# Optimization experiments

Measured on AMD Instinct MI355X. Metric: run time of the kernel, lower is better.

The kernel has to match this reference:

```python
import jax, jax.numpy as jnp
import numpy as np

EPS_F = 1e-6   # epsilon_F global in original repo
GAMMA = 0.8
K = 5
BN_EPS = 1e-5
M = 128
N = 100000
E = 1600000
MY = 10

def setup_inputs() -> dict:
    key = jax.random.key(0)
    ks = jax.random.split(key, 6)
    X = jax.random.normal(ks[0], (M, N), dtype=jnp.float32)
    # xavier_uniform for F: limit = sqrt(6/(m+m))
    lim = float(np.sqrt(6.0 / (M + M)))
    F_mat = jax.random.uniform(ks[1], (M, M), dtype=jnp.float32, minval=-lim, maxval=lim)
    B = (1.0 / np.sqrt(M)) * jax.random.normal(ks[2], (MY, M), dtype=jnp.float32)
    bn_weight = jnp.ones((M,), dtype=jnp.float32)
    bn_bias = jnp.zeros((M,), dtype=jnp.float32)
    edge_val = jax.random.uniform(ks[3], (E,), dtype=jnp.float32)
    edge_row = jax.random.randint(ks[4], (E,), 0, N, dtype=jnp.int64 if jax.config.jax_enable_x64 else jnp.int32)
    edge_col = jax.random.randint(ks[5], (E,), 0, N, dtype=jnp.int64 if jax.config.jax_enable_x64 else jnp.int32)
    return {"X": X, "F_mat": F_mat, "B": B, "bn_weight": bn_weight,
            "bn_bias": bn_bias, "edge_val": edge_val,
            "edge_row": edge_row, "edge_col": edge_col}

def reference(X, F_mat, B, bn_weight, bn_bias, edge_val, edge_row, edge_col):
    n = X.shape[1]
    # normalized Gram matrix g(F) = F^T F / (||F^T F||_fro + eps)
    FF = F_mat.T @ F_mat                       # [m, m]
    G = FF / (jnp.linalg.norm(FF) + EPS_F)
    X_first = X                                # [m, n]

    def step(Xc, _):
        Y = Xc.T                               # [n, m]
        # SpMM: (S_t @ Y)[r] += val * Y[c]
        SY = jax.ops.segment_sum(edge_val[:, None] * Y[edge_col], edge_row,
                                 num_segments=n)   # [n, m]
        Xn = GAMMA * (G @ SY.T) + X_first          # [m, n]
        return Xn, None

    Xk, _ = jax.lax.scan(step, X, None, length=K)
    out = Xk.T                                 # [n, m]
    # BatchNorm1d over feature dim (training-mode batch stats); dropout omitted (eval)
    mu = out.mean(axis=0)
    var = out.var(axis=0)
    out = (out - mu) * jax.lax.rsqrt(var + BN_EPS) * bn_weight + bn_bias
    return out @ B.T                           # [n, m_y]
```

## Files before the change

kernel.cpp:

```cpp
#include <hip/hip_runtime.h>
#include <math.h>

#define MDIM 128
#define MY 10
#define GAMMA 0.8f
#define KITER 5
#define NPASS 8

__device__ __forceinline__ float bf2f(unsigned short h) {
    return __uint_as_float(((unsigned int)h) << 16);
}
__device__ __forceinline__ unsigned short f2bf(float f) {
    unsigned int u = __float_as_uint(f);
    u += 0x7fffu + ((u >> 16) & 1u);
    return (unsigned short)(u >> 16);
}

__global__ void k_transpose(const float* __restrict__ X, float* __restrict__ Y0,
                            unsigned short* __restrict__ Y0h,
                            unsigned short* __restrict__ Yh0, int n) {
    __shared__ float tile[32][33];
    int r0 = blockIdx.x * 32;
    int f0 = blockIdx.y * 32;
    int tx = threadIdx.x, ty = threadIdx.y;
    #pragma unroll
    for (int i = 0; i < 32; i += 8) {
        tile[ty + i][tx] = X[(size_t)(f0 + ty + i) * n + (r0 + tx)];
    }
    __syncthreads();
    #pragma unroll
    for (int i = 0; i < 32; i += 8) {
        float v = tile[tx][ty + i];
        unsigned short h = f2bf(v);
        Y0[(size_t)(r0 + ty + i) * MDIM + (f0 + tx)] = v;
        Y0h[(size_t)(r0 + ty + i) * MDIM + (f0 + tx)] = h;
        Yh0[(size_t)(r0 + ty + i) * MDIM + (f0 + tx)] = h;
    }
}

__global__ void k_gram(const float* __restrict__ F, float* __restrict__ FF,
                       float* __restrict__ normAcc) {
    int i = blockIdx.x, j = threadIdx.x;
    float acc = 0.f;
    for (int k = 0; k < MDIM; ++k)
        acc = fmaf(F[k * MDIM + i], F[k * MDIM + j], acc);
    FF[i * MDIM + j] = acc;
    __shared__ float red[MDIM];
    red[j] = acc * acc;
    __syncthreads();
    for (int s = 64; s > 0; s >>= 1) {
        if (j < s) red[j] += red[j + s];
        __syncthreads();
    }
    if (j == 0) atomicAdd(normAcc, red[0]);
}

__global__ void k_gnorm(const float* __restrict__ FF, const float* __restrict__ normAcc,
                        float* __restrict__ G) {
    int idx = blockIdx.x * 256 + threadIdx.x;
    float s = GAMMA / (sqrtf(*normAcc) + 1e-6f);
    G[idx] = FF[idx] * s;
}

__global__ void k_hist(const int* __restrict__ erow, int* __restrict__ cnt, int E) {
    int e = blockIdx.x * 256 + threadIdx.x;
    if (e < E) atomicAdd(&cnt[erow[e]], 1);
}

__global__ void k_scan1(const int* __restrict__ cnt, int* __restrict__ blockSums, int n) {
    int tid = threadIdx.x;
    int base = blockIdx.x * 1024 + tid * 4;
    int s = 0;
    if (base + 3 < n) {
        int4 v = *(const int4*)&cnt[base];
        s = v.x + v.y + v.z + v.w;
    } else {
        for (int i = 0; i < 4; ++i)
            if (base + i < n) s += cnt[base + i];
    }
    __shared__ int red[256];
    red[tid] = s;
    __syncthreads();
    for (int st = 128; st > 0; st >>= 1) {
        if (tid < st) red[tid] += red[tid + st];
        __syncthreads();
    }
    if (tid == 0) blockSums[blockIdx.x] = red[0];
}

__global__ void k_scan2(int* __restrict__ blockSums, int* __restrict__ row_off,
                        int nb, int n) {
    __shared__ int s[256];
    int tid = threadIdx.x;
    int v = (tid < nb) ? blockSums[tid] : 0;
    s[tid] = v;
    __syncthreads();
    for (int off = 1; off < 256; off <<= 1) {
        int t = (tid >= off) ? s[tid - off] : 0;
        __syncthreads();
        s[tid] += t;
        __syncthreads();
    }
    if (tid < nb) blockSums[tid] = s[tid] - v;
    if (tid == 0) row_off[n] = s[255];
}

__global__ void k_scan3(const int* __restrict__ cnt, const int* __restrict__ blockOff,
                        int* __restrict__ row_off, int n) {
    int tid = threadIdx.x;
    int base = blockIdx.x * 1024 + tid * 4;
    int v[4];
    #pragma unroll
    for (int i = 0; i < 4; ++i) v[i] = (base + i < n) ? cnt[base + i] : 0;
    int local = v[0] + v[1] + v[2] + v[3];
    __shared__ int s[256];
    s[tid] = local;
    __syncthreads();
    for (int off = 1; off < 256; off <<= 1) {
        int t = (tid >= off) ? s[tid - off] : 0;
        __syncthreads();
        s[tid] += t;
        __syncthreads();
    }
    int excl = s[tid] - local + blockOff[blockIdx.x];
    #pragma unroll
    for (int i = 0; i < 4; ++i) {
        if (base + i < n) { row_off[base + i] = excl; excl += v[i]; }
    }
}

__global__ void k_scatter(const int* __restrict__ erow, const int* __restrict__ ecol,
                          const float* __restrict__ eval_, int* __restrict__ cursor,
                          int2* __restrict__ csr_cv, int E, int rlo, int rhi) {
    int e = blockIdx.x * 256 + threadIdx.x;
    if (e < E) {
        int r = erow[e];
        if (r >= rlo && r < rhi) {
            int pos = atomicAdd(&cursor[r], 1);
            csr_cv[pos] = make_int2(ecol[e] << 8, __float_as_int(eval_[e]));
        }
    }
}

__global__ void __launch_bounds__(256, 8) k_fused(const unsigned short* __restrict__ Yh,
                                                  const int* __restrict__ row_off,
                                                  const int2* __restrict__ csr_cv,
                                                  const float* __restrict__ G,
                                                  const float* __restrict__ Y0,
                                                  const unsigned short* __restrict__ Y0h,
                                                  float* __restrict__ Yout,
                                                  unsigned short* __restrict__ Yhout,
                                                  float* __restrict__ stats,
                                                  int writeH, int writeF, int n) {
    __shared__ float sSY[32 * MDIM];
    int tid = threadIdx.x;
    int ty = tid >> 5;
    int tx = tid & 31;
    int rbase = blockIdx.x * 32;
    const char* yb = (const char*)Yh;
    int lbo = tx * 8;

    for (int i = 0; i < 4; ++i) {
        int rloc = ty * 4 + i;
        int e0 = row_off[rbase + rloc];
        int e1 = row_off[rbase + rloc + 1];
        float4 a = make_float4(0.f, 0.f, 0.f, 0.f);
        int e = e0;
        for (; e + 8 <= e1; e += 8) {
            int2 p0 = csr_cv[e + 0];
            int2 p1 = csr_cv[e + 1];
            int2 p2 = csr_cv[e + 2];
            int2 p3 = csr_cv[e + 3];
            int2 p4 = csr_cv[e + 4];
            int2 p5 = csr_cv[e + 5];
            int2 p6 = csr_cv[e + 6];
            int2 p7 = csr_cv[e + 7];
            ushort4 h0 = *(const ushort4*)(yb + (size_t)(p0.x + lbo));
            ushort4 h1 = *(const ushort4*)(yb + (size_t)(p1.x + lbo));
            ushort4 h2 = *(const ushort4*)(yb + (size_t)(p2.x + lbo));
            ushort4 h3 = *(const ushort4*)(yb + (size_t)(p3.x + lbo));
            ushort4 h4 = *(const ushort4*)(yb + (size_t)(p4.x + lbo));
            ushort4 h5 = *(const ushort4*)(yb + (size_t)(p5.x + lbo));
            ushort4 h6 = *(const ushort4*)(yb + (size_t)(p6.x + lbo));
            ushort4 h7 = *(const ushort4*)(yb + (size_t)(p7.x + lbo));
            float v0 = __int_as_float(p0.y);
            float v1 = __int_as_float(p1.y);
            float v2 = __int_as_float(p2.y);
            float v3 = __int_as_float(p3.y);
            float v4 = __int_as_float(p4.y);
            float v5 = __int_as_float(p5.y);
            float v6 = __int_as_float(p6.y);
            float v7 = __int_as_float(p7.y);
            a.x = fmaf(v0, bf2f(h0.x), a.x);
            a.y = fmaf(v0, bf2f(h0.y), a.y);
            a.z = fmaf(v0, bf2f(h0.z), a.z);
            a.w = fmaf(v0, bf2f(h0.w), a.w);
            a.x = fmaf(v1, bf2f(h1.x), a.x);
            a.y = fmaf(v1, bf2f(h1.y), a.y);
            a.z = fmaf(v1, bf2f(h1.z), a.z);
            a.w = fmaf(v1, bf2f(h1.w), a.w);
            a.x = fmaf(v2, bf2f(h2.x), a.x);
            a.y = fmaf(v2, bf2f(h2.y), a.y);
            a.z = fmaf(v2, bf2f(h2.z), a.z);
            a.w = fmaf(v2, bf2f(h2.w), a.w);
            a.x = fmaf(v3, bf2f(h3.x), a.x);
            a.y = fmaf(v3, bf2f(h3.y), a.y);
            a.z = fmaf(v3, bf2f(h3.z), a.z);
            a.w = fmaf(v3, bf2f(h3.w), a.w);
            a.x = fmaf(v4, bf2f(h4.x), a.x);
            a.y = fmaf(v4, bf2f(h4.y), a.y);
            a.z = fmaf(v4, bf2f(h4.z), a.z);
            a.w = fmaf(v4, bf2f(h4.w), a.w);
            a.x = fmaf(v5, bf2f(h5.x), a.x);
            a.y = fmaf(v5, bf2f(h5.y), a.y);
            a.z = fmaf(v5, bf2f(h5.z), a.z);
            a.w = fmaf(v5, bf2f(h5.w), a.w);
            a.x = fmaf(v6, bf2f(h6.x), a.x);
            a.y = fmaf(v6, bf2f(h6.y), a.y);
            a.z = fmaf(v6, bf2f(h6.z), a.z);
            a.w = fmaf(v6, bf2f(h6.w), a.w);
            a.x = fmaf(v7, bf2f(h7.x), a.x);
            a.y = fmaf(v7, bf2f(h7.y), a.y);
            a.z = fmaf(v7, bf2f(h7.z), a.z);
            a.w = fmaf(v7, bf2f(h7.w), a.w);
        }
        for (; e + 4 <= e1; e += 4) {
            int2 p0 = csr_cv[e + 0];
            int2 p1 = csr_cv[e + 1];
            int2 p2 = csr_cv[e + 2];
            int2 p3 = csr_cv[e + 3];
            ushort4 h0 = *(const ushort4*)(yb + (size_t)(p0.x + lbo));
            ushort4 h1 = *(const ushort4*)(yb + (size_t)(p1.x + lbo));
            ushort4 h2 = *(const ushort4*)(yb + (size_t)(p2.x + lbo));
            ushort4 h3 = *(const ushort4*)(yb + (size_t)(p3.x + lbo));
            float v0 = __int_as_float(p0.y);
            float v1 = __int_as_float(p1.y);
            float v2 = __int_as_float(p2.y);
            float v3 = __int_as_float(p3.y);
            a.x = fmaf(v0, bf2f(h0.x), a.x);
            a.y = fmaf(v0, bf2f(h0.y), a.y);
            a.z = fmaf(v0, bf2f(h0.z), a.z);
            a.w = fmaf(v0, bf2f(h0.w), a.w);
            a.x = fmaf(v1, bf2f(h1.x), a.x);
            a.y = fmaf(v1, bf2f(h1.y), a.y);
            a.z = fmaf(v1, bf2f(h1.z), a.z);
            a.w = fmaf(v1, bf2f(h1.w), a.w);
            a.x = fmaf(v2, bf2f(h2.x), a.x);
            a.y = fmaf(v2, bf2f(h2.y), a.y);
            a.z = fmaf(v2, bf2f(h2.z), a.z);
            a.w = fmaf(v2, bf2f(h2.w), a.w);
            a.x = fmaf(v3, bf2f(h3.x), a.x);
            a.y = fmaf(v3, bf2f(h3.y), a.y);
            a.z = fmaf(v3, bf2f(h3.z), a.z);
            a.w = fmaf(v3, bf2f(h3.w), a.w);
        }
        for (; e < e1; ++e) {
            int2 p = csr_cv[e];
            float v = __int_as_float(p.y);
            ushort4 h = *(const ushort4*)(yb + (size_t)(p.x + lbo));
            a.x = fmaf(v, bf2f(h.x), a.x);
            a.y = fmaf(v, bf2f(h.y), a.y);
            a.z = fmaf(v, bf2f(h.z), a.z);
            a.w = fmaf(v, bf2f(h.w), a.w);
        }
        *(float4*)&sSY[rloc * MDIM + tx * 4] = a;
    }

    size_t r0 = (size_t)rbase + ty * 4;
    int f0 = tx * 4;
    float4 acc[4];
    #pragma unroll
    for (int i = 0; i < 4; ++i) acc[i] = make_float4(0.f, 0.f, 0.f, 0.f);

    for (int j = 0; j < MDIM; j += 4) {
        float4 g0 = *(const float4*)&G[(j + 0) * MDIM + f0];
        float4 g1 = *(const float4*)&G[(j + 1) * MDIM + f0];
        float4 g2 = *(const float4*)&G[(j + 2) * MDIM + f0];
        float4 g3 = *(const float4*)&G[(j + 3) * MDIM + f0];
        #pragma unroll
        for (int i = 0; i < 4; ++i) {
            float4 sr = *(const float4*)&sSY[(ty * 4 + i) * MDIM + j];
            acc[i].x = fmaf(sr.x, g0.x, acc[i].x);
            acc[i].y = fmaf(sr.x, g0.y, acc[i].y);
            acc[i].z = fmaf(sr.x, g0.z, acc[i].z);
            acc[i].w = fmaf(sr.x, g0.w, acc[i].w);
            acc[i].x = fmaf(sr.y, g1.x, acc[i].x);
            acc[i].y = fmaf(sr.y, g1.y, acc[i].y);
            acc[i].z = fmaf(sr.y, g1.z, acc[i].z);
            acc[i].w = fmaf(sr.y, g1.w, acc[i].w);
            acc[i].x = fmaf(sr.z, g2.x, acc[i].x);
            acc[i].y = fmaf(sr.z, g2.y, acc[i].y);
            acc[i].z = fmaf(sr.z, g2.z, acc[i].z);
            acc[i].w = fmaf(sr.z, g2.w, acc[i].w);
            acc[i].x = fmaf(sr.w, g3.x, acc[i].x);
            acc[i].y = fmaf(sr.w, g3.y, acc[i].y);
            acc[i].z = fmaf(sr.w, g3.z, acc[i].z);
            acc[i].w = fmaf(sr.w, g3.w, acc[i].w);
        }
    }

    float4 bs = make_float4(0.f, 0.f, 0.f, 0.f);
    float4 bq = make_float4(0.f, 0.f, 0.f, 0.f);
    #pragma unroll
    for (int i = 0; i < 4; ++i) {
        float4 y0;
        if (writeF) {
            y0 = *(const float4*)&Y0[(r0 + i) * MDIM + f0];
        } else {
            ushort4 t = *(const ushort4*)&Y0h[(r0 + i) * MDIM + f0];
            y0.x = bf2f(t.x);
            y0.y = bf2f(t.y);
            y0.z = bf2f(t.z);
            y0.w = bf2f(t.w);
        }
        float4 o;
        o.x = acc[i].x + y0.x;
        o.y = acc[i].y + y0.y;
        o.z = acc[i].z + y0.z;
        o.w = acc[i].w + y0.w;
        if (writeF) {
            *(float4*)&Yout[(r0 + i) * MDIM + f0] = o;
            bs.x += o.x; bs.y += o.y; bs.z += o.z; bs.w += o.w;
            bq.x = fmaf(o.x, o.x, bq.x);
            bq.y = fmaf(o.y, o.y, bq.y);
            bq.z = fmaf(o.z, o.z, bq.z);
            bq.w = fmaf(o.w, o.w, bq.w);
        }
        if (writeH) {
            ushort4 h;
            h.x = f2bf(o.x);
            h.y = f2bf(o.y);
            h.z = f2bf(o.z);
            h.w = f2bf(o.w);
            *(ushort4*)&Yhout[(r0 + i) * MDIM + f0] = h;
        }
    }

    if (writeF) {
        __syncthreads();
        *(float4*)&sSY[ty * MDIM + f0] = bs;
        *(float4*)&sSY[8 * MDIM + ty * MDIM + f0] = bq;
        __syncthreads();
        if (tid < MDIM) {
            float a = 0.f, b = 0.f;
            #pragma unroll
            for (int t = 0; t < 8; ++t) {
                a += sSY[t * MDIM + tid];
                b += sSY[8 * MDIM + t * MDIM + tid];
            }
            atomicAdd(&stats[tid], a);
            atomicAdd(&stats[MDIM + tid], b);
        }
    }
}

__global__ void k_finalize(const float* __restrict__ stats, const float* __restrict__ B,
                           const float* __restrict__ bnw, const float* __restrict__ bnb,
                           float* __restrict__ Bs, float* __restrict__ cvec, int n) {
    int f = threadIdx.x;
    float inv_n = 1.f / (float)n;
    float mu = stats[f] * inv_n;
    float var = stats[MDIM + f] * inv_n - mu * mu;
    float rs = rsqrtf(var + 1e-5f);
    float sw = rs * bnw[f];
    float cv = bnb[f] - mu * sw;
    __shared__ float red[MDIM];
    for (int o = 0; o < MY; ++o) {
        float b = B[o * MDIM + f];
        Bs[o * MDIM + f] = b * sw;
        red[f] = b * cv;
        __syncthreads();
        for (int s = 64; s > 0; s >>= 1) {
            if (f < s) red[f] += red[f + s];
            __syncthreads();
        }
        if (f == 0) cvec[o] = red[0];
        __syncthreads();
    }
}

__global__ void __launch_bounds__(256) k_project(const float* __restrict__ Y,
                                                 const float* __restrict__ Bs,
                                                 const float* __restrict__ cvec,
                                                 float* __restrict__ out, int n) {
    __shared__ float yt[16 * 129];
    __shared__ float sB[MY * 129];
    __shared__ float sc[MY];
    int tid = threadIdx.x;
    size_t rbase = (size_t)blockIdx.x * 16;
    for (int idx = tid; idx < 16 * MDIM; idx += 256) {
        int r = idx >> 7, f = idx & 127;
        yt[r * 129 + f] = Y[(rbase + r) * MDIM + f];
    }
    for (int idx = tid; idx < MY * MDIM; idx += 256) {
        int o = idx >> 7, f = idx & 127;
        sB[o * 129 + f] = Bs[idx];
    }
    if (tid < MY) sc[tid] = cvec[tid];
    __syncthreads();
    if (tid < 16 * MY) {
        int r = tid / MY, o = tid % MY;
        float acc = sc[o];
        for (int f = 0; f < MDIM; ++f)
            acc = fmaf(yt[r * 129 + f], sB[o * 129 + f], acc);
        out[(rbase + r) * MY + o] = acc;
    }
}

extern "C" void kernel_launch(void* const* d_in, const int* in_sizes, int n_in,
                              void* d_out, int out_size, void* d_ws, size_t ws_size,
                              hipStream_t stream) {
    const float* X    = (const float*)d_in[0];
    const float* F    = (const float*)d_in[1];
    const float* B    = (const float*)d_in[2];
    const float* bnw  = (const float*)d_in[3];
    const float* bnb  = (const float*)d_in[4];
    const float* ev   = (const float*)d_in[5];
    const int*   erow = (const int*)d_in[6];
    const int*   ecol = (const int*)d_in[7];
    float* out = (float*)d_out;
    const int n = in_sizes[0] / MDIM;
    const int E = in_sizes[5];

    char* w = (char*)d_ws;
    size_t off = 0;
    auto carve = [&](size_t bytes) -> void* {
        void* p = w + off;
        off += (bytes + 255) & ~(size_t)255;
        return p;
    };
    float*          Y0    = (float*)carve((size_t)n * MDIM * 4);
    float*          Ycur  = (float*)carve((size_t)n * MDIM * 4);
    unsigned short* Y0h   = (unsigned short*)carve((size_t)n * MDIM * 2);
    unsigned short* Yh_a  = (unsigned short*)carve((size_t)n * MDIM * 2);
    unsigned short* Yh_b  = (unsigned short*)carve((size_t)n * MDIM * 2);
    float* FF        = (float*)carve(MDIM * MDIM * 4);
    float* G         = (float*)carve(MDIM * MDIM * 4);
    int2*  csr_cv    = (int2*)carve((size_t)E * 8);
    int*   row_off   = (int*)carve((size_t)(n + 1) * 4);
    int*   cursor    = (int*)carve((size_t)n * 4);
    int*   cnt       = (int*)carve((size_t)n * 4);
    int*   blockSums = (int*)carve(1024 * 4);
    float* normAcc   = (float*)carve(4);
    float* stats     = (float*)carve(2 * MDIM * 4);
    float* Bs        = (float*)carve(MY * MDIM * 4);
    float* cvec      = (float*)carve(MY * 4);
    (void)ws_size;

    hipMemsetAsync(cnt, 0, (size_t)n * 4, stream);
    hipMemsetAsync(normAcc, 0, 4, stream);
    hipMemsetAsync(stats, 0, 2 * MDIM * 4, stream);

    k_transpose<<<dim3(n / 32, MDIM / 32), dim3(32, 8), 0, stream>>>(X, Y0, Y0h, Yh_a, n);
    k_gram<<<MDIM, MDIM, 0, stream>>>(F, FF, normAcc);
    k_gnorm<<<MDIM * MDIM / 256, 256, 0, stream>>>(FF, normAcc, G);

    const int nb = (n + 1023) / 1024;
    k_hist<<<(E + 255) / 256, 256, 0, stream>>>(erow, cnt, E);
    k_scan1<<<nb, 256, 0, stream>>>(cnt, blockSums, n);
    k_scan2<<<1, 256, 0, stream>>>(blockSums, row_off, nb, n);
    k_scan3<<<nb, 256, 0, stream>>>(cnt, blockSums, row_off, n);
    hipMemcpyAsync(cursor, row_off, (size_t)n * 4, hipMemcpyDeviceToDevice, stream);
    const int rstep = (n + NPASS - 1) / NPASS;
    for (int p = 0; p < NPASS; ++p) {
        int rlo = p * rstep;
        int rhi = rlo + rstep;
        if (rhi > n) rhi = n;
        k_scatter<<<(E + 255) / 256, 256, 0, stream>>>(erow, ecol, ev, cursor,
                                                       csr_cv, E, rlo, rhi);
    }

    for (int k = 0; k < KITER; ++k) {
        const unsigned short* hin = (k & 1) ? Yh_b : Yh_a;
        unsigned short*       hout = (k & 1) ? Yh_a : Yh_b;
        int writeH = (k < KITER - 1) ? 1 : 0;
        int writeF = (k == KITER - 1) ? 1 : 0;
        k_fused<<<n / 32, 256, 0, stream>>>(hin, row_off, csr_cv, G, Y0, Y0h, Ycur, hout,
                                            stats, writeH, writeF, n);
    }

    k_finalize<<<1, MDIM, 0, stream>>>(stats, B, bnw, bnb, Bs, cvec, n);
    k_project<<<n / 16, 256, 0, stream>>>(Ycur, Bs, cvec, out, n);
}
```

Baseline: 929.5 us.

## Replace multi-pass CSR scatter with two-level bucketed scatter

The CSR build used to run eight full passes over all edges, each placing only the edges whose row falls in a range. It now does one bucketing pass into 128-row buckets in a staging buffer, then a per-bucket placement kernel that writes final CSR positions from a localized range. This removes seven redundant reads of the edge arrays and should make the final scattered writes more cache-local. The cost is an extra staging buffer of E int2 and heavy atomic traffic on the bucket cursors. The fused kernel's grid size also changes to a ceiling division.

```diff
diff --git a/kernel.cpp b/kernel.cpp
--- a/kernel.cpp
+++ b/kernel.cpp
@@ -5,7 +5,8 @@
 #define MY 10
 #define GAMMA 0.8f
 #define KITER 5
-#define NPASS 8
+#define BSHIFT 7
+#define NBUCK(n) (((n) + 127) >> 7)
 
 __device__ __forceinline__ float bf2f(unsigned short h) {
     return __uint_as_float(((unsigned int)h) << 16);
@@ -129,16 +130,40 @@
     }
 }
 
-__global__ void k_scatter(const int* __restrict__ erow, const int* __restrict__ ecol,
-                          const float* __restrict__ eval_, int* __restrict__ cursor,
-                          int2* __restrict__ csr_cv, int E, int rlo, int rhi) {
+__global__ void k_binit(const int* __restrict__ row_off, int* __restrict__ bucketBase,
+                        int* __restrict__ bucketCursor, int nbk, int n) {
+    int b = blockIdx.x * 256 + threadIdx.x;
+    if (b <= nbk) {
+        int r = b << BSHIFT;
+        if (r > n) r = n;
+        int v = row_off[r];
+        bucketBase[b] = v;
+        if (b < nbk) bucketCursor[b] = v;
+    }
+}
+
+__global__ void k_bucket(const int* __restrict__ erow, const int* __restrict__ ecol,
+                         const float* __restrict__ eval_, int* __restrict__ bucketCursor,
+                         int2* __restrict__ stage, int E) {
     int e = blockIdx.x * 256 + threadIdx.x;
     if (e < E) {
         int r = erow[e];
-        if (r >= rlo && r < rhi) {
-            int pos = atomicAdd(&cursor[r], 1);
-            csr_cv[pos] = make_int2(ecol[e] << 8, __float_as_int(eval_[e]));
-        }
+        int c = ecol[e];
+        int pos = atomicAdd(&bucketCursor[r >> BSHIFT], 1);
+        stage[pos] = make_int2((c << BSHIFT) | (r & 127), __float_as_int(eval_[e]));
+    }
+}
+
+__global__ void k_place(const int2* __restrict__ stage, const int* __restrict__ bucketBase,
+                        int* __restrict__ cursor, int2* __restrict__ csr_cv) {
+    int b = blockIdx.x;
+    int lo = bucketBase[b], hi = bucketBase[b + 1];
+    int rbase = b << BSHIFT;
+    for (int e = lo + threadIdx.x; e < hi; e += 256) {
+        int2 s = stage[e];
+        int r = rbase + (s.x & 127);
+        int pos = atomicAdd(&cursor[r], 1);
+        csr_cv[pos] = make_int2((s.x >> BSHIFT) << 8, s.y);
     }
 }
 
@@ -307,11 +332,11 @@
         if (writeF) {
             y0 = *(const float4*)&Y0[(r0 + i) * MDIM + f0];
         } else {
-            ushort4 t = *(const ushort4*)&Y0h[(r0 + i) * MDIM + f0];
-            y0.x = bf2f(t.x);
-            y0.y = bf2f(t.y);
-            y0.z = bf2f(t.z);
-            y0.w = bf2f(t.w);
+            ushort4 t4 = *(const ushort4*)&Y0h[(r0 + i) * MDIM + f0];
+            y0.x = bf2f(t4.x);
+            y0.y = bf2f(t4.y);
+            y0.z = bf2f(t4.z);
+            y0.w = bf2f(t4.w);
         }
         float4 o;
         o.x = acc[i].x + y0.x;
@@ -421,6 +446,7 @@
     float* out = (float*)d_out;
     const int n = in_sizes[0] / MDIM;
     const int E = in_sizes[5];
+    const int nbk = NBUCK(n);
 
     char* w = (char*)d_ws;
     size_t off = 0;
@@ -437,10 +463,13 @@
     float* FF        = (float*)carve(MDIM * MDIM * 4);
     float* G         = (float*)carve(MDIM * MDIM * 4);
     int2*  csr_cv    = (int2*)carve((size_t)E * 8);
+    int2*  stage     = (int2*)carve((size_t)E * 8);
     int*   row_off   = (int*)carve((size_t)(n + 1) * 4);
     int*   cursor    = (int*)carve((size_t)n * 4);
     int*   cnt       = (int*)carve((size_t)n * 4);
     int*   blockSums = (int*)carve(1024 * 4);
+    int*   bucketBase   = (int*)carve((size_t)(nbk + 1) * 4);
+    int*   bucketCursor = (int*)carve((size_t)nbk * 4);
     float* normAcc   = (float*)carve(4);
     float* stats     = (float*)carve(2 * MDIM * 4);
     float* Bs        = (float*)carve(MY * MDIM * 4);
@@ -460,23 +489,18 @@
     k_scan1<<<nb, 256, 0, stream>>>(cnt, blockSums, n);
     k_scan2<<<1, 256, 0, stream>>>(blockSums, row_off, nb, n);
     k_scan3<<<nb, 256, 0, stream>>>(cnt, blockSums, row_off, n);
+    k_binit<<<(nbk + 256) / 256, 256, 0, stream>>>(row_off, bucketBase, bucketCursor, nbk, n);
     hipMemcpyAsync(cursor, row_off, (size_t)n * 4, hipMemcpyDeviceToDevice, stream);
-    const int rstep = (n + NPASS - 1) / NPASS;
-    for (int p = 0; p < NPASS; ++p) {
-        int rlo = p * rstep;
-        int rhi = rlo + rstep;
-        if (rhi > n) rhi = n;
-        k_scatter<<<(E + 255) / 256, 256, 0, stream>>>(erow, ecol, ev, cursor,
-                                                       csr_cv, E, rlo, rhi);
-    }
+    k_bucket<<<(E + 255) / 256, 256, 0, stream>>>(erow, ecol, ev, bucketCursor, stage, E);
+    k_place<<<nbk, 256, 0, stream>>>(stage, bucketBase, cursor, csr_cv);
 
     for (int k = 0; k < KITER; ++k) {
         const unsigned short* hin = (k & 1) ? Yh_b : Yh_a;
         unsigned short*       hout = (k & 1) ? Yh_a : Yh_b;
         int writeH = (k < KITER - 1) ? 1 : 0;
         int writeF = (k == KITER - 1) ? 1 : 0;
-        k_fused<<<n / 32, 256, 0, stream>>>(hin, row_off, csr_cv, G, Y0, Y0h, Ycur, hout,
-                                            stats, writeH, writeF, n);
+        k_fused<<<(n + 31) / 32, 256, 0, stream>>>(hin, row_off, csr_cv, G, Y0, Y0h,
+                                                   Ycur, hout, stats, writeH, writeF, n);
     }
 
     k_finalize<<<1, MDIM, 0, stream>>>(stats, B, bnw, bnb, Bs, cvec, n);
```

Measured after the change: 1.243 ms. 1.34x slower.

## Single-pass CSR scatter, drop fp32 output buffer, project from bf16, nontemporal edge loads

Applied to the files above, without the earlier changes.

Replaces the eight range-filtered scatter passes with one scatter pass and initializes the cursor inside the scan kernel, removing the device copy. The final iteration no longer writes an fp32 output; the projection reads the bf16 buffer instead. Edge-list loads in the SpMM use nontemporal hints. This cuts repeated edge reads and output traffic, at the cost of bf16 precision in the projection input and less locality in scatter atomics.

```diff
diff --git a/kernel.cpp b/kernel.cpp
--- a/kernel.cpp
+++ b/kernel.cpp
@@ -5,7 +5,6 @@
 #define MY 10
 #define GAMMA 0.8f
 #define KITER 5
-#define NPASS 8
 
 __device__ __forceinline__ float bf2f(unsigned short h) {
     return __uint_as_float(((unsigned int)h) << 16);
@@ -14,6 +13,13 @@
     unsigned int u = __float_as_uint(f);
     u += 0x7fffu + ((u >> 16) & 1u);
     return (unsigned short)(u >> 16);
+}
+__device__ __forceinline__ int2 ldnt(const int2* p) {
+    long long v = __builtin_nontemporal_load((const long long*)p);
+    int2 r;
+    r.x = (int)(v & 0xFFFFFFFFLL);
+    r.y = (int)(v >> 32);
+    return r;
 }
 
 __global__ void k_transpose(const float* __restrict__ X, float* __restrict__ Y0,
@@ -106,7 +112,7 @@
 }
 
 __global__ void k_scan3(const int* __restrict__ cnt, const int* __restrict__ blockOff,
-                        int* __restrict__ row_off, int n) {
+                        int* __restrict__ row_off, int* __restrict__ cursor, int n) {
     int tid = threadIdx.x;
     int base = blockIdx.x * 1024 + tid * 4;
     int v[4];
@@ -125,20 +131,23 @@
     int excl = s[tid] - local + blockOff[blockIdx.x];
     #pragma unroll
     for (int i = 0; i < 4; ++i) {
-        if (base + i < n) { row_off[base + i] = excl; excl += v[i]; }
+        if (base + i < n) {
+            row_off[base + i] = excl;
+            cursor[base + i] = excl;
+            excl += v[i];
+        }
     }
 }
 
 __global__ void k_scatter(const int* __restrict__ erow, const int* __restrict__ ecol,
                           const float* __restrict__ eval_, int* __restrict__ cursor,
-                          int2* __restrict__ csr_cv, int E, int rlo, int rhi) {
+                          int2* __restrict__ csr_cv, int E) {
     int e = blockIdx.x * 256 + threadIdx.x;
     if (e < E) {
         int r = erow[e];
-        if (r >= rlo && r < rhi) {
-            int pos = atomicAdd(&cursor[r], 1);
-            csr_cv[pos] = make_int2(ecol[e] << 8, __float_as_int(eval_[e]));
-        }
+        int c = ecol[e];
+        int pos = atomicAdd(&cursor[r], 1);
+        csr_cv[pos] = make_int2(c << 8, __float_as_int(eval_[e]));
     }
 }
 
@@ -148,10 +157,9 @@
                                                   const float* __restrict__ G,
                                                   const float* __restrict__ Y0,
                                                   const unsigned short* __restrict__ Y0h,
-                                                  float* __restrict__ Yout,
                                                   unsigned short* __restrict__ Yhout,
                                                   float* __restrict__ stats,
-                                                  int writeH, int writeF, int n) {
+                                                  int writeF, int n) {
     __shared__ float sSY[32 * MDIM];
     int tid = threadIdx.x;
     int ty = tid >> 5;
@@ -167,14 +175,14 @@
         float4 a = make_float4(0.f, 0.f, 0.f, 0.f);
         int e = e0;
         for (; e + 8 <= e1; e += 8) {
-            int2 p0 = csr_cv[e + 0];
-            int2 p1 = csr_cv[e + 1];
-            int2 p2 = csr_cv[e + 2];
-            int2 p3 = csr_cv[e + 3];
-            int2 p4 = csr_cv[e + 4];
-            int2 p5 = csr_cv[e + 5];
-            int2 p6 = csr_cv[e + 6];
-            int2 p7 = csr_cv[e + 7];
+            int2 p0 = ldnt(&csr_cv[e + 0]);
+            int2 p1 = ldnt(&csr_cv[e + 1]);
+            int2 p2 = ldnt(&csr_cv[e + 2]);
+            int2 p3 = ldnt(&csr_cv[e + 3]);
+            int2 p4 = ldnt(&csr_cv[e + 4]);
+            int2 p5 = ldnt(&csr_cv[e + 5]);
+            int2 p6 = ldnt(&csr_cv[e + 6]);
+            int2 p7 = ldnt(&csr_cv[e + 7]);
             ushort4 h0 = *(const ushort4*)(yb + (size_t)(p0.x + lbo));
             ushort4 h1 = *(const ushort4*)(yb + (size_t)(p1.x + lbo));
             ushort4 h2 = *(const ushort4*)(yb + (size_t)(p2.x + lbo));
@@ -225,10 +233,10 @@
             a.w = fmaf(v7, bf2f(h7.w), a.w);
         }
         for (; e + 4 <= e1; e += 4) {
-            int2 p0 = csr_cv[e + 0];
-            int2 p1 = csr_cv[e + 1];
-            int2 p2 = csr_cv[e + 2];
-            int2 p3 = csr_cv[e + 3];
+            int2 p0 = ldnt(&csr_cv[e + 0]);
+            int2 p1 = ldnt(&csr_cv[e + 1]);
+            int2 p2 = ldnt(&csr_cv[e + 2]);
+            int2 p3 = ldnt(&csr_cv[e + 3]);
             ushort4 h0 = *(const ushort4*)(yb + (size_t)(p0.x + lbo));
             ushort4 h1 = *(const ushort4*)(yb + (size_t)(p1.x + lbo));
             ushort4 h2 = *(const ushort4*)(yb + (size_t)(p2.x + lbo));
@@ -255,7 +263,7 @@
             a.w = fmaf(v3, bf2f(h3.w), a.w);
         }
         for (; e < e1; ++e) {
-            int2 p = csr_cv[e];
+            int2 p = ldnt(&csr_cv[e]);
             float v = __int_as_float(p.y);
             ushort4 h = *(const ushort4*)(yb + (size_t)(p.x + lbo));
             a.x = fmaf(v, bf2f(h.x), a.x);
@@ -307,11 +315,11 @@
         if (writeF) {
             y0 = *(const float4*)&Y0[(r0 + i) * MDIM + f0];
         } else {
-            ushort4 t = *(const ushort4*)&Y0h[(r0 + i) * MDIM + f0];
-            y0.x = bf2f(t.x);
-            y0.y = bf2f(t.y);
-            y0.z = bf2f(t.z);
-            y0.w = bf2f(t.w);
+            ushort4 t4 = *(const ushort4*)&Y0h[(r0 + i) * MDIM + f0];
+            y0.x = bf2f(t4.x);
+            y0.y = bf2f(t4.y);
+            y0.z = bf2f(t4.z);
+            y0.w = bf2f(t4.w);
         }
         float4 o;
         o.x = acc[i].x + y0.x;
@@ -319,21 +327,18 @@
         o.z = acc[i].z + y0.z;
         o.w = acc[i].w + y0.w;
         if (writeF) {
-            *(float4*)&Yout[(r0 + i) * MDIM + f0] = o;
             bs.x += o.x; bs.y += o.y; bs.z += o.z; bs.w += o.w;
             bq.x = fmaf(o.x, o.x, bq.x);
             bq.y = fmaf(o.y, o.y, bq.y);
             bq.z = fmaf(o.z, o.z, bq.z);
             bq.w = fmaf(o.w, o.w, bq.w);
         }
-        if (writeH) {
-            ushort4 h;
-            h.x = f2bf(o.x);
-            h.y = f2bf(o.y);
-            h.z = f2bf(o.z);
-            h.w = f2bf(o.w);
-            *(ushort4*)&Yhout[(r0 + i) * MDIM + f0] = h;
-        }
+        ushort4 h;
+        h.x = f2bf(o.x);
+        h.y = f2bf(o.y);
+        h.z = f2bf(o.z);
+        h.w = f2bf(o.w);
+        *(ushort4*)&Yhout[(r0 + i) * MDIM + f0] = h;
     }
 
     if (writeF) {
@@ -379,7 +384,7 @@
     }
 }
 
-__global__ void __launch_bounds__(256) k_project(const float* __restrict__ Y,
+__global__ void __launch_bounds__(256) k_project(const unsigned short* __restrict__ Yh,
                                                  const float* __restrict__ Bs,
                                                  const float* __restrict__ cvec,
                                                  float* __restrict__ out, int n) {
@@ -388,9 +393,14 @@
     __shared__ float sc[MY];
     int tid = threadIdx.x;
     size_t rbase = (size_t)blockIdx.x * 16;
-    for (int idx = tid; idx < 16 * MDIM; idx += 256) {
-        int r = idx >> 7, f = idx & 127;
-        yt[r * 129 + f] = Y[(rbase + r) * MDIM + f];
+    for (int idx = tid; idx < 16 * MDIM / 4; idx += 256) {
+        int r = idx >> 5;
+        int f = (idx & 31) * 4;
+        ushort4 h = *(const ushort4*)&Yh[(rbase + r) * MDIM + f];
+        yt[r * 129 + f + 0] = bf2f(h.x);
+        yt[r * 129 + f + 1] = bf2f(h.y);
+        yt[r * 129 + f + 2] = bf2f(h.z);
+        yt[r * 129 + f + 3] = bf2f(h.w);
     }
     for (int idx = tid; idx < MY * MDIM; idx += 256) {
         int o = idx >> 7, f = idx & 127;
@@ -430,7 +440,6 @@
         return p;
     };
     float*          Y0    = (float*)carve((size_t)n * MDIM * 4);
-    float*          Ycur  = (float*)carve((size_t)n * MDIM * 4);
     unsigned short* Y0h   = (unsigned short*)carve((size_t)n * MDIM * 2);
     unsigned short* Yh_a  = (unsigned short*)carve((size_t)n * MDIM * 2);
     unsigned short* Yh_b  = (unsigned short*)carve((size_t)n * MDIM * 2);
@@ -459,26 +468,18 @@
     k_hist<<<(E + 255) / 256, 256, 0, stream>>>(erow, cnt, E);
     k_scan1<<<nb, 256, 0, stream>>>(cnt, blockSums, n);
     k_scan2<<<1, 256, 0, stream>>>(blockSums, row_off, nb, n);
-    k_scan3<<<nb, 256, 0, stream>>>(cnt, blockSums, row_off, n);
-    hipMemcpyAsync(cursor, row_off, (size_t)n * 4, hipMemcpyDeviceToDevice, stream);
-    const int rstep = (n + NPASS - 1) / NPASS;
-    for (int p = 0; p < NPASS; ++p) {
-        int rlo = p * rstep;
-        int rhi = rlo + rstep;
-        if (rhi > n) rhi = n;
-        k_scatter<<<(E + 255) / 256, 256, 0, stream>>>(erow, ecol, ev, cursor,
-                                                       csr_cv, E, rlo, rhi);
-    }
+    k_scan3<<<nb, 256, 0, stream>>>(cnt, blockSums, row_off, cursor, n);
+    k_scatter<<<(E + 255) / 256, 256, 0, stream>>>(erow, ecol, ev, cursor, csr_cv, E);
 
     for (int k = 0; k < KITER; ++k) {
         const unsigned short* hin = (k & 1) ? Yh_b : Yh_a;
         unsigned short*       hout = (k & 1) ? Yh_a : Yh_b;
-        int writeH = (k < KITER - 1) ? 1 : 0;
         int writeF = (k == KITER - 1) ? 1 : 0;
-        k_fused<<<n / 32, 256, 0, stream>>>(hin, row_off, csr_cv, G, Y0, Y0h, Ycur, hout,
-                                            stats, writeH, writeF, n);
-    }
-
+        k_fused<<<(n + 31) / 32, 256, 0, stream>>>(hin, row_off, csr_cv, G, Y0, Y0h,
+                                                   hout, stats, writeF, n);
+    }
+
+    const unsigned short* Yfinal = (KITER & 1) ? Yh_b : Yh_a;
     k_finalize<<<1, MDIM, 0, stream>>>(stats, B, bnw, bnb, Bs, cvec, n);
-    k_project<<<n / 16, 256, 0, stream>>>(Ycur, Bs, cvec, out, n);
-}
+    k_project<<<n / 16, 256, 0, stream>>>(Yfinal, Bs, cvec, out, n);
+}
```

New measurement: 1.008 ms. 8.5% more time.
